# Optimization experiments

Hardware: AMD Instinct MI355X
Metric: run time of the kernel (lower is better)

Reference implementation:

```python
import jax, jax.numpy as jnp
import numpy as np

E, D, H, T = 8, 1024, 4096, 8192


def setup_inputs() -> dict:
    key = jax.random.key(0)
    k1, k2, k3 = jax.random.split(key, 3)
    inp = jax.random.normal(k1, (T, D), dtype=jnp.float32)
    w1 = jax.random.normal(k2, (E, H, D), dtype=jnp.float32) * (D ** -0.5)
    b1 = jnp.zeros((E, H), dtype=jnp.float32)
    w2 = jax.random.normal(k3, (E, D, H), dtype=jnp.float32) * (H ** -0.5)
    b2 = jnp.zeros((E, D), dtype=jnp.float32)
    fwd_expert_count = jnp.full((E,), T // E, dtype=jnp.int32)
    return {"inp": inp, "w1": w1, "b1": b1, "w2": w2, "b2": b2,
            "fwd_expert_count": fwd_expert_count}


def _grouped_linear(x, w, b, eid):
    # x: [T, in], w: [E, out, in], b: [E, out], eid: [T] expert id per token.
    # Tokens are contiguous per expert; we compute each expert's GEMM and
    # mask-select the rows belonging to that expert (small fixed E loop).
    out = jnp.zeros((x.shape[0], w.shape[1]), dtype=x.dtype)
    for e in range(w.shape[0]):
        mask = (eid == e)[:, None]
        out = out + jnp.where(mask, x @ w[e].T + b[e], jnp.zeros((), x.dtype))
    return out


def reference(inp, w1, b1, w2, b2, fwd_expert_count):
    # Map each (sorted) token to its expert via cumulative segment bounds.
    bounds = jnp.cumsum(fwd_expert_count)            # [E]
    eid = jnp.searchsorted(bounds, jnp.arange(inp.shape[0]), side="right")  # [T]
    h = _grouped_linear(inp, w1, b1, eid)            # [T, H]  itoh
    h = jax.nn.gelu(h, approximate=False)            # activation
    out = _grouped_linear(h, w2, b2, eid)            # [T, D]  htoi
    return out
```

## Files before the change

### kernel.cpp

```cpp
#include <hip/hip_runtime.h>
#include <hip/hip_bf16.h>
#include <cstdint>
#include <cstddef>


typedef __bf16 bf16x8 __attribute__((ext_vector_type(8)));
typedef float f32x4 __attribute__((ext_vector_type(4)));
typedef unsigned short u16x8 __attribute__((ext_vector_type(8)));

#define BM 128
#define BN 128

__device__ __forceinline__ unsigned short f2bf(float f) {
  unsigned u = __builtin_bit_cast(unsigned, f);
  u += 0x7FFFu + ((u >> 16) & 1u);
  return (unsigned short)(u >> 16);
}

__device__ __forceinline__ float fast_gelu(float v) {
  const float u = 0.7978845608028654f * (v + 0.044715f * v * v * v);
  const float t = 1.0f - 2.0f / (__expf(2.0f * u) + 1.0f);
  return 0.5f * v * (1.0f + t);
}

__device__ __forceinline__ void gload16(const void* g, void* lds) {
  __builtin_amdgcn_global_load_lds(
      (const __attribute__((address_space(1))) void*)g,
      (__attribute__((address_space(3))) void*)lds, 16, 0, 0);
}

__device__ __forceinline__ void cvt8(const float* __restrict__ src,
                                     unsigned short* __restrict__ dst, long i) {
  float4 a = *reinterpret_cast<const float4*>(src + i);
  float4 b = *reinterpret_cast<const float4*>(src + i + 4);
  u16x8 o;
  o[0] = f2bf(a.x); o[1] = f2bf(a.y); o[2] = f2bf(a.z); o[3] = f2bf(a.w);
  o[4] = f2bf(b.x); o[5] = f2bf(b.y); o[6] = f2bf(b.z); o[7] = f2bf(b.w);
  *reinterpret_cast<u16x8*>(dst + i) = o;
}

__global__ void cvt2_build(const float* __restrict__ s0,
                           unsigned short* __restrict__ d0, long n0,
                           const float* __restrict__ s1,
                           unsigned short* __restrict__ d1, long n1,
                           const int* __restrict__ cnt, int E,
                           int4* __restrict__ tbl, int* __restrict__ ntp) {
  if (blockIdx.x == 0 && threadIdx.x == 0) {
    int nt = 0, start = 0;
    for (int e = 0; e < E; ++e) {
      int c = cnt[e];
      for (int t = 0; t < c; t += BM) {
        int4 v; v.x = e; v.y = start + t; v.z = (c - t < BM ? c - t : BM); v.w = 0;
        tbl[nt++] = v;
      }
      start += c;
    }
    *ntp = nt;
  }
  long i = ((long)blockIdx.x * blockDim.x + threadIdx.x) * 8;
  const long stride = (long)gridDim.x * blockDim.x * 8;
  const long ntot = n0 + n1;
  for (; i < ntot; i += stride) {
    if (i < n0) cvt8(s0, d0, i);
    else        cvt8(s1, d1, i - n0);
  }
}

template <int GELU, int OUTBF, int PIGGY, int SINGLEA, int WPE>
__global__ __launch_bounds__(256, WPE) void grouped_gemm(
    const unsigned short* __restrict__ A, const unsigned short* __restrict__ W,
    const float* __restrict__ bias, void* __restrict__ Cv,
    const int4* __restrict__ tbl, const int* __restrict__ ntp,
    const int N, const int K,
    const float* __restrict__ pg_src, unsigned short* __restrict__ pg_dst,
    const long pg_n, const int yTiles) {
  constexpr int BKT = 64;
  if (PIGGY && (int)blockIdx.y >= yTiles) {
    const int p = ((int)blockIdx.y - yTiles) * gridDim.x + blockIdx.x;
    const long PB = (long)(gridDim.y - yTiles) * gridDim.x;
    long i = ((long)p * blockDim.x + threadIdx.x) * 8;
    const long stride = PB * blockDim.x * 8;
    for (; i < pg_n; i += stride) cvt8(pg_src, pg_dst, i);
    return;
  }

  const int mt = blockIdx.y;
  const int bx = blockIdx.x;
  if (mt >= *ntp) return;
  const int4 ti = tbl[mt];
  const int e = ti.x, row0 = ti.y, rows = ti.z;
  const int bcol = bx * BN;

  constexpr int SABUF = SINGLEA ? 1 : 2;
  __shared__ alignas(16) unsigned short raw[(SABUF + 2) * BM * BKT];
  auto sA = [&](int b) { return &raw[b * BM * BKT]; };
  auto sB = [&](int b) { return &raw[(SABUF + b) * BN * BKT]; };

  const int tid = threadIdx.x;
  const int lane = tid & 63;
  const int wave = tid >> 6;
  const int wr = wave >> 1;
  const int wc = wave & 1;
  const int lr = lane & 15;
  const int lhi = lane >> 4;

  const unsigned short* __restrict__ Wexp = W + (size_t)e * N * K;

  constexpr int CH  = BKT / 8;
  constexpr int LPM = BKT / 16;
  constexpr int RPL = 2048 / BKT;
  const int srow = wave * 8 + (lane >> 3);
  const int chn = lane & (CH - 1);
  const int cg = chn ^ (srow & (CH - 1));

  const unsigned short* gA[LPM];
  const unsigned short* gB[LPM];
#pragma unroll
  for (int i = 0; i < LPM; ++i) {
    const int rA = srow + i * RPL;
    const int rc = rA < rows ? rA : rows - 1;
    gA[i] = A + (size_t)(row0 + rc) * K + cg * 8;
    gB[i] = Wexp + (size_t)(bcol + srow + i * RPL) * K + cg * 8;
  }

  auto stage = [&](int kt, int bA, int bB) {
    char* da = (char*)sA(bA) + wave * 1024;
    char* db = (char*)sB(bB) + wave * 1024;
#pragma unroll
    for (int i = 0; i < LPM; ++i) {
      gload16(gA[i] + kt * BKT, da + i * 4096);
      gload16(gB[i] + kt * BKT, db + i * 4096);
    }
  };

  constexpr int KH = BKT / 32;
  int swo[KH];
#pragma unroll
  for (int kh = 0; kh < KH; ++kh)
    swo[kh] = ((kh * 4 + lhi) ^ (lr & (CH - 1))) * 8;
  const int aRowB = wr * 64 + lr;
  const int bRowB = wc * 64 + lr;

  f32x4 acc[4][4] = {};
  const int nk = K / BKT;

  stage(0, 0, 0);
  __syncthreads();

  int buf = 0;
  if constexpr (SINGLEA) {
    for (int t = 0; t < nk; ++t) {
      bf16x8 af[4][KH], bfr[4][KH];
#pragma unroll
      for (int m = 0; m < 4; ++m) {
        const unsigned short* rp = &sA(0)[(aRowB + m * 16) * BKT];
#pragma unroll
        for (int kh = 0; kh < KH; ++kh)
          af[m][kh] = *reinterpret_cast<const bf16x8*>(rp + swo[kh]);
      }
#pragma unroll
      for (int n = 0; n < 4; ++n) {
        const unsigned short* rp = &sB(buf)[(bRowB + n * 16) * BKT];
#pragma unroll
        for (int kh = 0; kh < KH; ++kh)
          bfr[n][kh] = *reinterpret_cast<const bf16x8*>(rp + swo[kh]);
      }
      __syncthreads();
      if (t + 1 < nk) stage(t + 1, 0, buf ^ 1);
#pragma unroll
      for (int kh = 0; kh < KH; ++kh)
#pragma unroll
        for (int m = 0; m < 4; ++m)
#pragma unroll
          for (int n = 0; n < 4; ++n)
            acc[m][n] = __builtin_amdgcn_mfma_f32_16x16x32_bf16(
                af[m][kh], bfr[n][kh], acc[m][n], 0, 0, 0);
      __syncthreads();
      buf ^= 1;
    }
  } else {
    for (int t = 0; t < nk; ++t) {
      if (t + 1 < nk) stage(t + 1, buf ^ 1, buf ^ 1);
#pragma unroll
      for (int kh = 0; kh < KH; ++kh) {
        bf16x8 af[4], bfr[4];
#pragma unroll
        for (int m = 0; m < 4; ++m)
          af[m] = *reinterpret_cast<const bf16x8*>(
              &sA(buf)[(aRowB + m * 16) * BKT + swo[kh]]);
#pragma unroll
        for (int n = 0; n < 4; ++n)
          bfr[n] = *reinterpret_cast<const bf16x8*>(
              &sB(buf)[(bRowB + n * 16) * BKT + swo[kh]]);
#pragma unroll
        for (int m = 0; m < 4; ++m)
#pragma unroll
          for (int n = 0; n < 4; ++n)
            acc[m][n] = __builtin_amdgcn_mfma_f32_16x16x32_bf16(
                af[m], bfr[n], acc[m][n], 0, 0, 0);
      }
      __syncthreads();
      buf ^= 1;
    }
  }

  const float* __restrict__ be = bias + (size_t)e * N;
  if constexpr (SINGLEA && OUTBF) {
    unsigned short* tb = raw;
#pragma unroll
    for (int n = 0; n < 4; ++n) {
      const int col = wc * 64 + n * 16 + lr;
      const float bv = be[bcol + col];
#pragma unroll
      for (int m = 0; m < 4; ++m) {
#pragma unroll
        for (int j = 0; j < 4; ++j) {
          const int row = wr * 64 + m * 16 + (lhi << 2) + j;
          float v = acc[m][n][j] + bv;
          if (GELU) v = fast_gelu(v);
          tb[row * BN + col] = f2bf(v);
        }
      }
    }
    __syncthreads();
    unsigned short* __restrict__ hout = (unsigned short*)Cv;
#pragma unroll
    for (int i = 0; i < 8; ++i) {
      const int flat = i * 256 + tid;
      const int row = flat >> 4;
      const int ch = flat & 15;
      if (row < rows)
        *reinterpret_cast<u16x8*>(&hout[(size_t)(row0 + row) * N + bcol + ch * 8]) =
            *reinterpret_cast<const u16x8*>(&tb[row * BN + ch * 8]);
    }
  } else {
    const int colBase = bcol + wc * 64 + lr;
    const int rowBase = wr * 64 + (lhi << 2);
#pragma unroll
    for (int n = 0; n < 4; ++n) {
      const int col = colBase + n * 16;
      const float bv = be[col];
#pragma unroll
      for (int m = 0; m < 4; ++m) {
        const int r0 = rowBase + m * 16;
#pragma unroll
        for (int j = 0; j < 4; ++j) {
          const int rr = r0 + j;
          if (rr < rows) {
            float v = acc[m][n][j] + bv;
            if (GELU) v = fast_gelu(v);
            const size_t idx = (size_t)(row0 + rr) * N + col;
            if (OUTBF) ((unsigned short*)Cv)[idx] = f2bf(v);
            else       ((float*)Cv)[idx] = v;
          }
        }
      }
    }
  }
}

extern "C" void kernel_launch(void* const* d_in, const int* in_sizes, int n_in,
                              void* d_out, int out_size, void* d_ws, size_t ws_size,
                              hipStream_t stream) {
  const float* inp = (const float*)d_in[0];
  const float* w1  = (const float*)d_in[1];
  const float* b1  = (const float*)d_in[2];
  const float* w2  = (const float*)d_in[3];
  const float* b2  = (const float*)d_in[4];
  const int*   cnt = (const int*)d_in[5];

  const int E = in_sizes[5];
  const int H = in_sizes[2] / E;
  const int D = in_sizes[4] / E;
  const int T = in_sizes[0] / D;

  char* ws = (char*)d_ws;
  int4* tbl = (int4*)ws;
  int* ntp = (int*)(ws + 2048);
  size_t off = 4096;
  unsigned short* inp_bf = (unsigned short*)(ws + off); off += (size_t)T * D * 2;
  unsigned short* w1_bf  = (unsigned short*)(ws + off); off += (size_t)E * H * D * 2;
  unsigned short* w2_bf  = (unsigned short*)(ws + off); off += (size_t)E * D * H * 2;
  unsigned short* h_bf   = (unsigned short*)(ws + off); off += (size_t)T * H * 2;
  (void)ws_size; (void)n_in; (void)out_size;

  cvt2_build<<<2048, 256, 0, stream>>>(inp, inp_bf, (long)T * D,
                                       w1, w1_bf, (long)E * H * D,
                                       cnt, E, tbl, ntp);

  const int maxTiles = T / BM + E;
  dim3 g1(H / BN, maxTiles + 8);
  grouped_gemm<1, 1, 1, 1, 3><<<g1, 256, 0, stream>>>(
      inp_bf, w1_bf, b1, h_bf, tbl, ntp, H, D,
      w2, w2_bf, (long)E * D * H, maxTiles);
  dim3 g2(D / BN, maxTiles);
  grouped_gemm<0, 0, 0, 0, 2><<<g2, 256, 0, stream>>>(
      h_bf, w2_bf, b2, d_out, tbl, ntp, D, H,
      nullptr, nullptr, 0, maxTiles);
}
```

Before: 267.6 us.

## Interleave w2 fp32-to-bf16 conversion into GEMM1 main loop instead of extra blocks

The separate piggyback blocks that converted w2 to bf16 after the GEMM tiles are removed. Instead, the first PIGF GEMM1 blocks each convert a slice of w2 inside their K loop, one 8-element chunk per thread per iteration, so the global loads and stores overlap with MFMA work. This aims to hide the conversion's memory traffic behind compute. The cost is extra registers and memory traffic in those blocks, which could make them stragglers and hurt occupancy.

```diff
diff --git a/kernel.cpp b/kernel.cpp
--- a/kernel.cpp
+++ b/kernel.cpp
@@ -73,17 +73,8 @@
     const int4* __restrict__ tbl, const int* __restrict__ ntp,
     const int N, const int K,
     const float* __restrict__ pg_src, unsigned short* __restrict__ pg_dst,
-    const long pg_n, const int yTiles) {
+    const long pg_n) {
   constexpr int BKT = 64;
-  if (PIGGY && (int)blockIdx.y >= yTiles) {
-    const int p = ((int)blockIdx.y - yTiles) * gridDim.x + blockIdx.x;
-    const long PB = (long)(gridDim.y - yTiles) * gridDim.x;
-    long i = ((long)p * blockDim.x + threadIdx.x) * 8;
-    const long stride = PB * blockDim.x * 8;
-    for (; i < pg_n; i += stride) cvt8(pg_src, pg_dst, i);
-    return;
-  }
-
   const int mt = blockIdx.y;
   const int bx = blockIdx.x;
   if (mt >= *ntp) return;
@@ -144,6 +135,31 @@
   f32x4 acc[4][4] = {};
   const int nk = K / BKT;
 
+  const int flat = mt * gridDim.x + bx;
+  const long pgUnits = pg_n >> 11;
+  const int PIGF = (int)((pgUnits + nk - 1) / nk);
+  const bool pig = (PIGGY == 2) && (flat < PIGF);
+  float4 pa, pb;
+  long pi = -1;
+  auto pigStore = [&]() {
+    if (pi >= 0) {
+      u16x8 o;
+      o[0] = f2bf(pa.x); o[1] = f2bf(pa.y); o[2] = f2bf(pa.z); o[3] = f2bf(pa.w);
+      o[4] = f2bf(pb.x); o[5] = f2bf(pb.y); o[6] = f2bf(pb.z); o[7] = f2bf(pb.w);
+      *reinterpret_cast<u16x8*>(pg_dst + pi) = o;
+    }
+  };
+  auto pigLoad = [&](int t) {
+    const long i = (((long)flat * nk + t) * 256 + tid) * 8;
+    if (i < pg_n) {
+      pa = *reinterpret_cast<const float4*>(pg_src + i);
+      pb = *reinterpret_cast<const float4*>(pg_src + i + 4);
+      pi = i;
+    } else {
+      pi = -1;
+    }
+  };
+
   stage(0, 0, 0);
   __syncthreads();
 
@@ -167,6 +183,7 @@
       }
       __syncthreads();
       if (t + 1 < nk) stage(t + 1, 0, buf ^ 1);
+      if (pig) { pigStore(); pigLoad(t); }
 #pragma unroll
       for (int kh = 0; kh < KH; ++kh)
 #pragma unroll
@@ -178,6 +195,7 @@
       __syncthreads();
       buf ^= 1;
     }
+    if (pig) pigStore();
   } else {
     for (int t = 0; t < nk; ++t) {
       if (t + 1 < nk) stage(t + 1, buf ^ 1, buf ^ 1);
@@ -226,9 +244,9 @@
     unsigned short* __restrict__ hout = (unsigned short*)Cv;
 #pragma unroll
     for (int i = 0; i < 8; ++i) {
-      const int flat = i * 256 + tid;
-      const int row = flat >> 4;
-      const int ch = flat & 15;
+      const int fl = i * 256 + tid;
+      const int row = fl >> 4;
+      const int ch = fl & 15;
       if (row < rows)
         *reinterpret_cast<u16x8*>(&hout[(size_t)(row0 + row) * N + bcol + ch * 8]) =
             *reinterpret_cast<const u16x8*>(&tb[row * BN + ch * 8]);
@@ -289,12 +307,12 @@
                                        cnt, E, tbl, ntp);
 
   const int maxTiles = T / BM + E;
-  dim3 g1(H / BN, maxTiles + 8);
-  grouped_gemm<1, 1, 1, 1, 3><<<g1, 256, 0, stream>>>(
+  dim3 g1(H / BN, maxTiles);
+  grouped_gemm<1, 1, 2, 1, 3><<<g1, 256, 0, stream>>>(
       inp_bf, w1_bf, b1, h_bf, tbl, ntp, H, D,
-      w2, w2_bf, (long)E * D * H, maxTiles);
+      w2, w2_bf, (long)E * D * H);
   dim3 g2(D / BN, maxTiles);
   grouped_gemm<0, 0, 0, 0, 2><<<g2, 256, 0, stream>>>(
       h_bf, w2_bf, b2, d_out, tbl, ntp, D, H,
-      nullptr, nullptr, 0, maxTiles);
-}
+      nullptr, nullptr, 0);
+}
```

Result: slower. 399.6 us (+49.3%).
